# Kernel optimization log

Hardware: AMD Instinct MI355X
Metric: run time of the kernel (lower is better)

The kernel has to match this reference:

```python
import jax, jax.numpy as jnp
import numpy as np

B, C, OC, H, W = 2, 64, 128, 96, 96
HD, DI, N, R, K = C // 2, C, 16, 2, 4  # VSSBlock: hidden=C/2, d_inner=2*hidden=C, d_state, dt_rank, 4 scan dirs
EPS = 1e-5


def _conv(x, w, b, pad, groups=1):
    y = jax.lax.conv_general_dilated(x, w, (1, 1), pad, feature_group_count=groups,
                                     dimension_numbers=('NCHW', 'OIHW', 'NCHW'))
    return y + b[None, :, None, None]


def _ln(x, w, b):
    m = x.mean(-1, keepdims=True)
    v = x.var(-1, keepdims=True)
    return (x - m) * jax.lax.rsqrt(v + EPS) * w + b


def _selective_scan(xs, dts, Bs, Cs, A, D):
    # xs, dts: (B,K,DI,L); Bs, Cs: (B,K,N,L); A: (K,DI,N); D: (K,DI)
    dts = jax.nn.softplus(dts)

    def step(h, inp):
        u_t, dt_t, B_t, C_t = inp
        dA = jnp.exp(dt_t[..., None] * A)                         # (B,K,DI,N)
        h = dA * h + (dt_t * u_t)[..., None] * B_t[:, :, None, :]
        return h, jnp.einsum('bkdn,bkn->bkd', h, C_t)

    seq = (jnp.moveaxis(xs, -1, 0), jnp.moveaxis(dts, -1, 0),
           jnp.moveaxis(Bs, -1, 0), jnp.moveaxis(Cs, -1, 0))
    h0 = jnp.zeros(xs.shape[:3] + (A.shape[-1],), xs.dtype)
    _, ys = jax.lax.scan(step, h0, seq)
    return jnp.moveaxis(ys, 0, -1) + D[None, :, :, None] * xs


def _vss_block(x, ln_w, ln_b, in_w, conv_w, conv_b, xproj_w, dtproj_w, dtproj_b,
               A_logs, Ds, on_w, on_b, out_w):
    # x: (B,H,W,HD); VMamba SS2D with 4-direction cross-scan + residual
    b, hh, ww, _ = x.shape
    L = hh * ww
    h = _ln(x, ln_w, ln_b)
    xz = h @ in_w                                   # (B,H,W,2*DI)
    xp, z = jnp.split(xz, 2, axis=-1)
    xc = jnp.transpose(xp, (0, 3, 1, 2))            # (B,DI,H,W)
    xc = jax.nn.silu(_conv(xc, conv_w, conv_b, ((1, 1), (1, 1)), groups=DI))
    x_flat = xc.reshape(b, DI, L)
    x_wh = jnp.transpose(xc, (0, 1, 3, 2)).reshape(b, DI, L)
    x2 = jnp.stack([x_flat, x_wh], axis=1)
    xs = jnp.concatenate([x2, jnp.flip(x2, -1)], axis=1)      # (B,4,DI,L)
    x_dbl = jnp.einsum('bkdl,kcd->bkcl', xs, xproj_w)
    dts, Bs, Cs = jnp.split(x_dbl, [R, R + N], axis=2)
    dts = jnp.einsum('bkrl,kdr->bkdl', dts, dtproj_w) + dtproj_b[None, :, :, None]
    A = -jnp.exp(A_logs)
    ys = _selective_scan(xs, dts, Bs, Cs, A, Ds)              # (B,4,DI,L)
    inv = jnp.flip(ys[:, 2:4], -1)
    unwh = lambda t: jnp.transpose(t.reshape(b, DI, ww, hh), (0, 1, 3, 2)).reshape(b, DI, L)
    y = ys[:, 0] + inv[:, 0] + unwh(ys[:, 1]) + unwh(inv[:, 1])
    y = jnp.transpose(y.reshape(b, DI, hh, ww), (0, 2, 3, 1))
    y = _ln(y, on_w, on_b) * jax.nn.silu(z)
    return x + y @ out_w


def _forward(x, ms_dw33_w, ms_dw33_b, ms_in_w, ms_in_b, ms_scale,
             vss_ln_w, vss_ln_b, vss_in_w, vss_conv_w, vss_conv_b, vss_xproj_w,
             vss_dtproj_w, vss_dtproj_b, vss_A_logs, vss_Ds, vss_on_w, vss_on_b, vss_out_w,
             ma_conv_w, ma_conv_b, adw_h_w, adw_h_b, adw_w_w, adw_w_b,
             pw_w, pw_b, bn_w, bn_b, bn_mean, bn_var):
    vss = (vss_ln_w, vss_ln_b, vss_in_w, vss_conv_w, vss_conv_b, vss_xproj_w,
           vss_dtproj_w, vss_dtproj_b, vss_A_logs, vss_Ds, vss_on_w, vss_on_b, vss_out_w)
    # --- MambaSplit (shared VSSBlock applied to both channel halves) ---
    xd = _conv(x, ms_dw33_w, ms_dw33_b, ((1, 1), (1, 1)), groups=C)
    x1, x2 = jnp.split(xd, 2, axis=1)

    def branch(xp):
        y = _vss_block(jnp.transpose(xp, (0, 2, 3, 1)), *vss)
        return ms_scale * xp + jnp.transpose(y, (0, 3, 1, 2))

    xm = jnp.concatenate([branch(x1), branch(x2)], axis=1)
    m = xm.mean((2, 3), keepdims=True)
    v = xm.var((2, 3), keepdims=True)
    xm = (xm - m) * jax.lax.rsqrt(v + EPS) * ms_in_w[None, :, None, None] + ms_in_b[None, :, None, None]
    xm = jax.nn.leaky_relu(xm, 0.01)
    # --- MaxAvg (global avg+max pool -> 3x3 conv on 1x1 map -> sigmoid gate) ---
    pooled = jnp.concatenate([x.mean((2, 3), keepdims=True), x.max((2, 3), keepdims=True)], axis=1)
    gate = jax.nn.sigmoid(_conv(pooled, ma_conv_w, ma_conv_b, ((1, 1), (1, 1))))
    xs_ = xm + gate * x
    # --- AxialDW ---
    xs_ = xs_ + _conv(xs_, adw_h_w, adw_h_b, ((1, 1), (0, 0)), groups=C) \
              + _conv(xs_, adw_w_w, adw_w_b, ((0, 0), (1, 1)), groups=C)
    # --- BN (eval) + ReLU, 1x1 conv, 2x2 maxpool ---
    skip = jax.nn.relu((xs_ - bn_mean[None, :, None, None]) * jax.lax.rsqrt(bn_var[None, :, None, None] + EPS)
                       * bn_w[None, :, None, None] + bn_b[None, :, None, None])
    out = _conv(skip, pw_w, pw_b, ((0, 0), (0, 0)))
    down = jax.lax.reduce_window(out, -jnp.inf, jax.lax.max, (1, 1, 2, 2), (1, 1, 2, 2), 'VALID')
    return down, skip


def setup_inputs() -> dict:
    key = jax.random.key(0)
    ks = jax.random.split(key, 16)
    r = lambda i, shape, s=0.02: jax.random.normal(ks[i], shape, jnp.float32) * s
    return {
        'x': jax.random.normal(ks[0], (B, C, H, W), jnp.float32),
        'ms_dw33_w': r(1, (C, 1, 3, 3), 0.1), 'ms_dw33_b': jnp.zeros(C),
        'ms_in_w': jnp.ones(C), 'ms_in_b': jnp.zeros(C),
        'ms_scale': jnp.ones((1,)),
        'vss_ln_w': jnp.ones(HD), 'vss_ln_b': jnp.zeros(HD),
        'vss_in_w': r(2, (HD, 2 * DI)),
        'vss_conv_w': r(3, (DI, 1, 3, 3), 0.1), 'vss_conv_b': jnp.zeros(DI),
        'vss_xproj_w': r(4, (K, R + 2 * N, DI)),
        'vss_dtproj_w': r(5, (K, DI, R), 0.1), 'vss_dtproj_b': r(6, (K, DI), 0.1),
        'vss_A_logs': jnp.tile(jnp.log(jnp.arange(1, N + 1, dtype=jnp.float32)), (K, DI, 1)),
        'vss_Ds': jnp.ones((K, DI)),
        'vss_on_w': jnp.ones(DI), 'vss_on_b': jnp.zeros(DI),
        'vss_out_w': r(7, (DI, HD)),
        'ma_conv_w': r(8, (C, 2 * C, 3, 3), 0.05), 'ma_conv_b': jnp.zeros(C),
        'adw_h_w': r(9, (C, 1, 3, 1), 0.1), 'adw_h_b': jnp.zeros(C),
        'adw_w_w': r(10, (C, 1, 1, 3), 0.1), 'adw_w_b': jnp.zeros(C),
        'pw_w': r(11, (OC, C, 1, 1)), 'pw_b': jnp.zeros(OC),
        'bn_w': jnp.ones(C), 'bn_b': jnp.zeros(C),
        'bn_mean': jnp.zeros(C), 'bn_var': jnp.ones(C),
    }


def reference(x, ms_dw33_w, ms_dw33_b, ms_in_w, ms_in_b, ms_scale,
              vss_ln_w, vss_ln_b, vss_in_w, vss_conv_w, vss_conv_b, vss_xproj_w,
              vss_dtproj_w, vss_dtproj_b, vss_A_logs, vss_Ds, vss_on_w, vss_on_b, vss_out_w,
              ma_conv_w, ma_conv_b, adw_h_w, adw_h_b, adw_w_w, adw_w_b,
              pw_w, pw_b, bn_w, bn_b, bn_mean, bn_var):
    return _forward(x, ms_dw33_w, ms_dw33_b, ms_in_w, ms_in_b, ms_scale,
                    vss_ln_w, vss_ln_b, vss_in_w, vss_conv_w, vss_conv_b, vss_xproj_w,
                    vss_dtproj_w, vss_dtproj_b, vss_A_logs, vss_Ds, vss_on_w, vss_on_b, vss_out_w,
                    ma_conv_w, ma_conv_b, adw_h_w, adw_h_b, adw_w_w, adw_w_b,
                    pw_w, pw_b, bn_w, bn_b, bn_mean, bn_var)
```

## Files before the change

kernel.cpp:

```cpp
#include <hip/hip_runtime.h>
#include <hip/hip_bf16.h>

typedef __hip_bfloat16 bf16;
#define DEV __device__ __forceinline__

constexpr int B_ = 2, C_ = 64, H_ = 96, W_ = 96, L_ = 9216;
constexpr int HD_ = 32, DI_ = 64, N_ = 16, K_ = 4, BB_ = 4;
constexpr int OC_ = 128;
constexpr int CH_ = 384, CL_ = 24;
constexpr int SEGN = 32, SEGC = 12;
constexpr float EPSF = 1e-5f;
constexpr int DOWN_SZ = B_ * OC_ * 48 * 48;

typedef __attribute__((ext_vector_type(8))) short short8;
typedef __attribute__((ext_vector_type(4))) float f32x4;
typedef __attribute__((ext_vector_type(2))) float f32x2;

DEV float softplusf(float x) { return x > 15.f ? x : __logf(1.f + __expf(x)); }
DEV float b2f(bf16 v) { return __bfloat162float(v); }
DEV float lo16f(unsigned v) { return __uint_as_float(v << 16); }
DEV float hi16f(unsigned v) { return __uint_as_float(v & 0xffff0000u); }
DEV f32x2 pk2(unsigned w) { f32x2 r = {lo16f(w), hi16f(w)}; return r; }
DEV void unpk8(uint4 a, float* v) {
  v[0] = lo16f(a.x); v[1] = hi16f(a.x); v[2] = lo16f(a.y); v[3] = hi16f(a.y);
  v[4] = lo16f(a.z); v[5] = hi16f(a.z); v[6] = lo16f(a.w); v[7] = hi16f(a.w);
}
DEV void unpk(uint4 a, uint4 b, float* v) {
  unpk8(a, v); unpk8(b, v + 8);
}

__constant__ float kLogN[16] = {
  0.0f, 0.69314718f, 1.09861229f, 1.38629436f, 1.60943791f, 1.79175947f,
  1.94591015f, 2.07944154f, 2.19722458f, 2.30258509f, 2.39789527f,
  2.48490665f, 2.56494936f, 2.63905733f, 2.70805020f, 2.77258872f};

DEV void pow_tree2(float e1, f32x2* ep) {
  float e2 = e1 * e1;
  ep[0].x = e1; ep[0].y = e2;
  f32x2 b2v = {e2, e2};
  ep[1] = ep[0] * b2v;
  float e4 = ep[1].y;
  f32x2 b4v = {e4, e4};
  ep[2] = ep[0] * b4v;
  ep[3] = ep[1] * b4v;
  float e8 = ep[3].y;
  f32x2 b8v = {e8, e8};
  ep[4] = ep[0] * b8v;
  ep[5] = ep[1] * b8v;
  ep[6] = ep[2] * b8v;
  ep[7] = ep[3] * b8v;
}

DEV void pow_tree(float e1, float* ep) {
  float e2 = e1 * e1, e4 = e2 * e2, e8 = e4 * e4;
  float e3 = e2 * e1, e5 = e4 * e1, e6 = e4 * e2, e7 = e4 * e3;
  ep[0] = e1;  ep[1] = e2;  ep[2] = e3;  ep[3] = e4;
  ep[4] = e5;  ep[5] = e6;  ep[6] = e7;  ep[7] = e8;
  ep[8] = e8 * e1;  ep[9] = e8 * e2;  ep[10] = e8 * e3;  ep[11] = e8 * e4;
  ep[12] = e8 * e5; ep[13] = e8 * e6; ep[14] = e8 * e7;  ep[15] = e8 * e8;
}

__global__ __launch_bounds__(256, 4) void k_front(
    const float* __restrict__ x, const float* __restrict__ dw33w,
    const float* __restrict__ dw33b, const float* __restrict__ lnw,
    const float* __restrict__ lnb, const float* __restrict__ inw,
    const float* __restrict__ xpw, const float* __restrict__ alog,
    float* __restrict__ xd, bf16* __restrict__ xzAh, bf16* __restrict__ xzBh,
    bf16* __restrict__ wh, float* __restrict__ aux) {
  int bb = blockIdx.y, t = threadIdx.x;
  int b = bb & 1, co = (bb >> 1) * HD_;
  int idx0 = blockIdx.x * 32;
  if (bb == 0) {
    int i = blockIdx.x * 256 + t;
    if (i < 144 * 64) {
      int n = i >> 6;
      wh[i] = __float2bfloat16(n < 136 ? xpw[i] : 0.f);
    }
    if (blockIdx.x == 0) {
      int kd = t;
      const float* al = alog + kd * N_;
      float a0 = al[0];
      bool lin = true;
#pragma unroll
      for (int n = 1; n < N_; n++) lin = lin && (fabsf(al[n] - a0 - kLogN[n]) < 3e-5f);
      aux[kd] = -__expf(a0);
      aux[256 + kd] = lin ? 1.f : 0.f;
#pragma unroll
      for (int n = 0; n < N_; n++) aux[512 + kd * N_ + n] = -__expf(al[n]);
    }
  }
  __shared__ float xds[32 * 36];
  __shared__ float meanA[32], rstdA[32];
  for (int i = t; i < 1024; i += 256) {
    int cl = i >> 5, ii = i & 31;
    int sp = idx0 + ii, wi = sp % 96, hi = sp / 96;
    int cg = b * C_ + co + cl;
    float acc = dw33b[co + cl];
#pragma unroll
    for (int dy = -1; dy <= 1; dy++) {
      int hh = hi + dy; if (hh < 0 || hh >= H_) continue;
#pragma unroll
      for (int dx = -1; dx <= 1; dx++) {
        int ww = wi + dx; if (ww < 0 || ww >= W_) continue;
        acc = fmaf(x[(size_t)cg * L_ + sp + dy * 96 + dx],
                   dw33w[(co + cl) * 9 + (dy + 1) * 3 + (dx + 1)], acc);
      }
    }
    xds[cl * 36 + ii] = acc;
    xd[(size_t)cg * L_ + sp] = acc;
  }
  __syncthreads();
  if (t < 32) {
    float s = 0.f, sq = 0.f;
#pragma unroll
    for (int c = 0; c < 32; c++) { float v = xds[c * 36 + t]; s += v; sq = fmaf(v, v, sq); }
    float mean = s * (1.f / HD_);
    float var = sq * (1.f / HD_) - mean * mean;
    meanA[t] = mean; rstdA[t] = rsqrtf(var + EPSF);
  }
  __syncthreads();
  for (int i = t; i < 1024; i += 256) {
    int c = i >> 5, idx = i & 31;
    float v = xds[c * 36 + idx];
    xds[c * 36 + idx] = (v - meanA[idx]) * rstdA[idx] * lnw[c] + lnb[c];
  }
  __syncthreads();
  int oc = t & 127, g = t >> 7;
  float acc[16];
#pragma unroll
  for (int j = 0; j < 16; j++) acc[j] = 0.f;
  for (int c = 0; c < 32; c++) {
    float wv = inw[c * 128 + oc];
    const float4* row = reinterpret_cast<const float4*>(&xds[c * 36 + g * 16]);
#pragma unroll
    for (int j4 = 0; j4 < 4; j4++) {
      float4 xv = row[j4];
      acc[j4 * 4 + 0] = fmaf(xv.x, wv, acc[j4 * 4 + 0]);
      acc[j4 * 4 + 1] = fmaf(xv.y, wv, acc[j4 * 4 + 1]);
      acc[j4 * 4 + 2] = fmaf(xv.z, wv, acc[j4 * 4 + 2]);
      acc[j4 * 4 + 3] = fmaf(xv.w, wv, acc[j4 * 4 + 3]);
    }
  }
  int occ = oc & 63;
  if (oc < 64) {
#pragma unroll
    for (int j = 0; j < 16; j++)
      xzAh[(size_t)(bb * L_ + idx0 + g * 16 + j) * 64 + occ] = __float2bfloat16(acc[j]);
  } else {
#pragma unroll
    for (int j = 0; j < 16; j++)
      xzBh[(size_t)(bb * L_ + idx0 + g * 16 + j) * 64 + occ] = __float2bfloat16(acc[j]);
  }
}

__global__ void k_dwsilu(const bf16* __restrict__ xzAh, const float* __restrict__ cw,
                         const float* __restrict__ cb, bf16* __restrict__ xch,
                         bf16* __restrict__ xcht) {
  int t = blockIdx.x * 256 + threadIdx.x;
  int d = t & 63, idx = (t >> 6) % L_, bb = t / (L_ * DI_);
  int wi = idx % W_, hi = idx / W_;
  float acc = cb[d];
#pragma unroll
  for (int dy = -1; dy <= 1; dy++) {
    int hh = hi + dy; if (hh < 0 || hh >= H_) continue;
#pragma unroll
    for (int dx = -1; dx <= 1; dx++) {
      int ww = wi + dx; if (ww < 0 || ww >= W_) continue;
      acc = fmaf(b2f(xzAh[(size_t)(bb * L_ + hh * W_ + ww) * 64 + d]),
                 cw[d * 9 + (dy + 1) * 3 + (dx + 1)], acc);
    }
  }
  acc = acc / (1.f + __expf(-acc));
  bf16 v = __float2bfloat16(acc);
  xch[t] = v;
  int idx_t = wi * 96 + hi;
  xcht[((size_t)bb * L_ + idx_t) * DI_ + d] = v;
}

__global__ __launch_bounds__(256, 4) void k_xdbl_mfma(
    const bf16* __restrict__ xch, const bf16* __restrict__ wh,
    float* __restrict__ xdblB, bf16* __restrict__ xdblC) {
  int w = threadIdx.x >> 6, lane = threadIdx.x & 63;
  int bb = blockIdx.y;
  int mtile = blockIdx.x * 4 + w;
  int idx0 = mtile * 16;
  int m = lane & 15, quad = lane >> 4;
  const bf16* arow = xch + ((size_t)bb * L_ + idx0 + m) * 64 + quad * 8;
  short8 a0 = *reinterpret_cast<const short8*>(arow);
  short8 a1 = *reinterpret_cast<const short8*>(arow + 32);
  int ntb = blockIdx.z * 3;
#pragma unroll
  for (int it = 0; it < 3; it++) {
    int nt = ntb + it;
    int n = nt * 16 + m;
    const bf16* brow = wh + n * 64 + quad * 8;
    short8 b0 = *reinterpret_cast<const short8*>(brow);
    short8 b1 = *reinterpret_cast<const short8*>(brow + 32);
    f32x4 acc = {0.f, 0.f, 0.f, 0.f};
    acc = __builtin_amdgcn_mfma_f32_16x16x32_bf16(a0, b0, acc, 0, 0, 0);
    acc = __builtin_amdgcn_mfma_f32_16x16x32_bf16(a1, b1, acc, 0, 0, 0);
    if (n < 136) {
      int k4 = (n >= 102) ? 3 : (n >= 68) ? 2 : (n >= 34) ? 1 : 0;
      int c = n - k4 * 34;
#pragma unroll
      for (int i = 0; i < 4; i++) {
        int r = idx0 + quad * 4 + i;
        int hi2 = r / 96, wi2 = r - hi2 * 96;
        int tr = wi2 * 96 + hi2;
        int ls = (k4 == 0) ? r : (k4 == 1) ? tr : (k4 == 2) ? (L_ - 1 - r) : (L_ - 1 - tr);
        size_t row = (size_t)(bb * K_ + k4) * L_ + ls;
        if (c < 2)       xdblB[row * 12 + 8 + c] = acc[i];
        else if (c < 18) ((bf16*)(xdblB + row * 12))[c - 2] = __float2bfloat16(acc[i]);
        else             xdblC[row * 16 + (c - 18)] = __float2bfloat16(acc[i]);
      }
    }
  }
}

__global__ __launch_bounds__(256, 4) void k_scan1(
    const float* __restrict__ xdblB, const bf16* __restrict__ xch,
    const bf16* __restrict__ xcht, const float* __restrict__ dtw,
    const float* __restrict__ dtb, const float* __restrict__ aux,
    bf16* __restrict__ hbuf, float* __restrict__ ssum) {
  int w = threadIdx.x >> 6, d = threadIdx.x & 63;
  int bx = blockIdx.x;
  int chunk = bx * 4 + w, k = blockIdx.y, bb = blockIdx.z;
  const float* bB = xdblB + (size_t)(bb * K_ + k) * L_ * 12;
  __shared__ __align__(16) float sB[96 * 12];
  {
    const uint4* src = (const uint4*)(bB + (size_t)bx * 96 * 12);
    uint4* dst = (uint4*)sB;
    for (int i = threadIdx.x; i < 288; i += 256) dst[i] = src[i];
  }
  __syncthreads();
  float w0 = dtw[(k * DI_ + d) * 2 + 0], w1 = dtw[(k * DI_ + d) * 2 + 1];
  float bia = dtb[k * DI_ + d];
  float A1 = aux[k * 64 + d];
  bool chain = (__ballot(aux[256 + k * 64 + d] > 0.5f) == ~0ull);
  const bf16* ub = ((k & 1) ? xcht : xch) + (size_t)bb * L_ * DI_;
  int ls0 = chunk * CL_;
  int uidx0 = (k & 2) ? (L_ - 1 - ls0) : ls0;
  int ustep = (k & 2) ? -1 : 1;
  float S = 0.f;
  size_t base = (size_t)((bb * K_ + k) * CH_ + chunk) * DI_ + d;
  if (chain) {
    f32x2 h2[8];
#pragma unroll
    for (int i = 0; i < 8; i++) { h2[i].x = 0.f; h2[i].y = 0.f; }
#pragma unroll 4
    for (int s = 0; s < CL_; s++) {
      const float* p = sB + (w * CL_ + s) * 12;
      uint4 qb0 = *(const uint4*)p, qb1 = *(const uint4*)(p + 4);
      float t0 = p[8], t1 = p[9];
      float u = b2f(ub[(size_t)(uidx0 + s * ustep) * DI_ + d]);
      float dt = softplusf(fmaf(t0, w0, fmaf(t1, w1, bia)));
      S += dt;
      float du = dt * u;
      f32x2 du2 = {du, du};
      f32x2 ep2[8];
      pow_tree2(__expf(dt * A1), ep2);
      h2[0] = ep2[0] * h2[0] + du2 * pk2(qb0.x);
      h2[1] = ep2[1] * h2[1] + du2 * pk2(qb0.y);
      h2[2] = ep2[2] * h2[2] + du2 * pk2(qb0.z);
      h2[3] = ep2[3] * h2[3] + du2 * pk2(qb0.w);
      h2[4] = ep2[4] * h2[4] + du2 * pk2(qb1.x);
      h2[5] = ep2[5] * h2[5] + du2 * pk2(qb1.y);
      h2[6] = ep2[6] * h2[6] + du2 * pk2(qb1.z);
      h2[7] = ep2[7] * h2[7] + du2 * pk2(qb1.w);
    }
#pragma unroll
    for (int i = 0; i < 8; i++) {
      hbuf[base * N_ + 2 * i]     = __float2bfloat16(h2[i].x);
      hbuf[base * N_ + 2 * i + 1] = __float2bfloat16(h2[i].y);
    }
  } else {
    float h[N_];
#pragma unroll
    for (int n = 0; n < N_; n++) h[n] = 0.f;
    float A[N_];
#pragma unroll
    for (int n = 0; n < N_; n++) A[n] = aux[512 + (k * 64 + d) * N_ + n];
    for (int s = 0; s < CL_; s++) {
      const float* p = sB + (w * CL_ + s) * 12;
      uint4 qb0 = *(const uint4*)p, qb1 = *(const uint4*)(p + 4);
      float t0 = p[8], t1 = p[9];
      float u = b2f(ub[(size_t)(uidx0 + s * ustep) * DI_ + d]);
      float Bv[16];
      unpk(qb0, qb1, Bv);
      float dt = softplusf(fmaf(t0, w0, fmaf(t1, w1, bia)));
      S += dt;
      float du = dt * u;
#pragma unroll
      for (int n = 0; n < N_; n++) h[n] = fmaf(__expf(dt * A[n]), h[n], du * Bv[n]);
    }
#pragma unroll
    for (int n = 0; n < N_; n++) hbuf[base * N_ + n] = __float2bfloat16(h[n]);
  }
  ssum[base] = S;
}

__global__ __launch_bounds__(256, 4) void k_scan2a(
    const float* __restrict__ aux, const float* __restrict__ ssum,
    bf16* __restrict__ hbuf, float* __restrict__ cumS,
    float* __restrict__ segH, float* __restrict__ segS) {
  int t = blockIdx.x * 256 + threadIdx.x;
  int n = t & 15, d = (t >> 4) & 63, kk = (t >> 10) & 3, bb = (t >> 12) & 3, seg = t >> 14;
  float A = aux[512 + (kk * 64 + d) * N_ + n];
  size_t row = (size_t)(bb * K_ + kk) * CH_ * DI_ + d;
  float hp = 0.f, Sc = 0.f;
#pragma unroll 4
  for (int j = 0; j < SEGC; j++) {
    int c = seg * SEGC + j;
    size_t sb = row + (size_t)c * DI_;
    float S = ssum[sb];
    float hl = b2f(hbuf[sb * N_ + n]);
    hbuf[sb * N_ + n] = __float2bfloat16(hp);
    if (n == 0) cumS[sb] = Sc;
    hp = fmaf(__expf(A * S), hp, hl);
    Sc += S;
  }
  size_t sbase = (size_t)(bb * K_ + kk) * SEGN + seg;
  segH[(sbase * DI_ + d) * N_ + n] = hp;
  if (n == 0) segS[sbase * DI_ + d] = Sc;
}

__global__ void k_scan2b(const float* __restrict__ aux, float* __restrict__ segH,
                         const float* __restrict__ segS) {
  int t = blockIdx.x * 256 + threadIdx.x;
  int n = t & 15, d = (t >> 4) & 63, kk = (t >> 10) & 3, bb = t >> 12;
  float A = aux[512 + (kk * 64 + d) * N_ + n];
  float hp = 0.f;
  for (int seg = 0; seg < SEGN; seg++) {
    size_t sbase = (size_t)(bb * K_ + kk) * SEGN + seg;
    size_t si = (sbase * DI_ + d) * N_ + n;
    float H = segH[si];
    float E = __expf(A * segS[sbase * DI_ + d]);
    segH[si] = hp;
    hp = fmaf(E, hp, H);
  }
}

__global__ __launch_bounds__(256, 4) void k_scan3(
    const float* __restrict__ xdblB, const bf16* __restrict__ xdblC,
    const bf16* __restrict__ xch, const bf16* __restrict__ xcht,
    const float* __restrict__ dtw, const float* __restrict__ dtb,
    const float* __restrict__ Dsw, const float* __restrict__ aux,
    const bf16* __restrict__ hbuf, const float* __restrict__ cumS,
    const float* __restrict__ segH, bf16* __restrict__ ydir) {
  int w = threadIdx.x >> 6, d = threadIdx.x & 63;
  int bx = blockIdx.x;
  int chunk = bx * 4 + w, k = blockIdx.y, bb = blockIdx.z;
  const float* bB = xdblB + (size_t)(bb * K_ + k) * L_ * 12;
  const bf16* bC = xdblC + (size_t)(bb * K_ + k) * L_ * 16;
  __shared__ __align__(16) float sB[96 * 12];
  __shared__ __align__(16) bf16 sC[96 * 16];
  {
    const uint4* srcB = (const uint4*)(bB + (size_t)bx * 96 * 12);
    uint4* dstB = (uint4*)sB;
    for (int i = threadIdx.x; i < 288; i += 256) dstB[i] = srcB[i];
    const uint4* srcC = (const uint4*)(bC + (size_t)bx * 96 * 16);
    uint4* dstC = (uint4*)sC;
    if (threadIdx.x < 192) dstC[threadIdx.x] = srcC[threadIdx.x];
  }
  __syncthreads();
  float w0 = dtw[(k * DI_ + d) * 2 + 0], w1 = dtw[(k * DI_ + d) * 2 + 1];
  float bia = dtb[k * DI_ + d];
  float Dk = Dsw[k * DI_ + d];
  float A1 = aux[k * 64 + d];
  bool chain = (__ballot(aux[256 + k * 64 + d] > 0.5f) == ~0ull);
  size_t base = (size_t)((bb * K_ + k) * CH_ + chunk) * DI_ + d;
  int seg = chunk / SEGC;
  size_t sbase = (size_t)(bb * K_ + k) * SEGN + seg;
  float Sc = cumS[base];
  const bf16* ub = ((k & 1) ? xcht : xch) + (size_t)bb * L_ * DI_;
  bf16* yb = ydir + (size_t)(bb * K_ + k) * L_ * DI_;
  int ls0 = chunk * CL_;
  int uidx0 = (k & 2) ? (L_ - 1 - ls0) : ls0;
  int ustep = (k & 2) ? -1 : 1;
  const bf16* hb = hbuf + base * N_;
  const float* Hin = segH + (sbase * DI_ + d) * N_;
  if (chain) {
    f32x2 h2[8];
    {
      uint4 qh0 = *(const uint4*)hb, qh1 = *(const uint4*)(hb + 8);
      h2[0] = pk2(qh0.x); h2[1] = pk2(qh0.y); h2[2] = pk2(qh0.z); h2[3] = pk2(qh0.w);
      h2[4] = pk2(qh1.x); h2[5] = pk2(qh1.y); h2[6] = pk2(qh1.z); h2[7] = pk2(qh1.w);
      f32x2 ep2[8];
      pow_tree2(__expf(A1 * Sc), ep2);
#pragma unroll
      for (int i = 0; i < 8; i++)
        h2[i] = ep2[i] * (*(const f32x2*)(Hin + 2 * i)) + h2[i];
    }
#pragma unroll 2
    for (int s = 0; s < CL_; s++) {
      int lr = w * CL_ + s;
      const float* p = sB + lr * 12;
      uint4 qb0 = *(const uint4*)p, qb1 = *(const uint4*)(p + 4);
      float t0 = p[8], t1 = p[9];
      const uint4* cq = (const uint4*)(sC + lr * 16);
      uint4 qc0 = cq[0], qc1 = cq[1];
      float u = b2f(ub[(size_t)(uidx0 + s * ustep) * DI_ + d]);
      float dt = softplusf(fmaf(t0, w0, fmaf(t1, w1, bia)));
      float du = dt * u;
      f32x2 du2 = {du, du};
      f32x2 ep2[8];
      pow_tree2(__expf(dt * A1), ep2);
      f32x2 y2 = {0.f, 0.f};
      h2[0] = ep2[0] * h2[0] + du2 * pk2(qb0.x);  y2 = h2[0] * pk2(qc0.x) + y2;
      h2[1] = ep2[1] * h2[1] + du2 * pk2(qb0.y);  y2 = h2[1] * pk2(qc0.y) + y2;
      h2[2] = ep2[2] * h2[2] + du2 * pk2(qb0.z);  y2 = h2[2] * pk2(qc0.z) + y2;
      h2[3] = ep2[3] * h2[3] + du2 * pk2(qb0.w);  y2 = h2[3] * pk2(qc0.w) + y2;
      h2[4] = ep2[4] * h2[4] + du2 * pk2(qb1.x);  y2 = h2[4] * pk2(qc1.x) + y2;
      h2[5] = ep2[5] * h2[5] + du2 * pk2(qb1.y);  y2 = h2[5] * pk2(qc1.y) + y2;
      h2[6] = ep2[6] * h2[6] + du2 * pk2(qb1.z);  y2 = h2[6] * pk2(qc1.z) + y2;
      h2[7] = ep2[7] * h2[7] + du2 * pk2(qb1.w);  y2 = h2[7] * pk2(qc1.w) + y2;
      float y = fmaf(Dk, u, y2.x + y2.y);
      yb[(size_t)(ls0 + s) * DI_ + d] = __float2bfloat16(y);
    }
  } else {
    float h[N_];
    {
      uint4 qh0 = *(const uint4*)hb, qh1 = *(const uint4*)(hb + 8);
      unpk(qh0, qh1, h);
#pragma unroll
      for (int n = 0; n < N_; n++) {
        float A = aux[512 + (k * 64 + d) * N_ + n];
        h[n] = fmaf(__expf(A * Sc), Hin[n], h[n]);
      }
    }
    float A[N_];
#pragma unroll
    for (int n = 0; n < N_; n++) A[n] = aux[512 + (k * 64 + d) * N_ + n];
    for (int s = 0; s < CL_; s++) {
      int lr = w * CL_ + s;
      const float* p = sB + lr * 12;
      uint4 qb0 = *(const uint4*)p, qb1 = *(const uint4*)(p + 4);
      float t0 = p[8], t1 = p[9];
      const uint4* cq = (const uint4*)(sC + lr * 16);
      uint4 qc0 = cq[0], qc1 = cq[1];
      float u = b2f(ub[(size_t)(uidx0 + s * ustep) * DI_ + d]);
      float Bv[16], Cv[16];
      unpk(qb0, qb1, Bv); unpk(qc0, qc1, Cv);
      float dt = softplusf(fmaf(t0, w0, fmaf(t1, w1, bia)));
      float du = dt * u;
      float y = 0.f;
#pragma unroll
      for (int n = 0; n < N_; n++) {
        h[n] = fmaf(__expf(dt * A[n]), h[n], du * Bv[n]);
        y = fmaf(h[n], Cv[n], y);
      }
      y = fmaf(Dk, u, y);
      yb[(size_t)(ls0 + s) * DI_ + d] = __float2bfloat16(y);
    }
  }
}

__global__ void k_combine(const bf16* __restrict__ ydir, const bf16* __restrict__ xzBh,
                          const float* __restrict__ xd, const float* __restrict__ onw,
                          const float* __restrict__ onb, const float* __restrict__ outw,
                          const float* __restrict__ mssc, float* __restrict__ xm) {
  int w = threadIdx.x >> 6, d = threadIdx.x & 63;
  int idx = blockIdx.x * 4 + w, bb = blockIdx.y;
  int b = bb & 1, co = (bb >> 1) * HD_;
  int hii = idx / 96, wii = idx - hii * 96;
  int lt = wii * 96 + hii;
  const bf16* yd = ydir + (size_t)bb * K_ * L_ * DI_;
  float y = b2f(yd[((size_t)0 * L_ + idx) * DI_ + d])
          + b2f(yd[((size_t)1 * L_ + lt) * DI_ + d])
          + b2f(yd[((size_t)2 * L_ + (L_ - 1 - idx)) * DI_ + d])
          + b2f(yd[((size_t)3 * L_ + (L_ - 1 - lt)) * DI_ + d]);
  float s = y, sq = y * y;
#pragma unroll
  for (int m = 1; m < 64; m <<= 1) { s += __shfl_xor(s, m, 64); sq += __shfl_xor(sq, m, 64); }
  float mean = s * (1.f / DI_);
  float var = sq * (1.f / DI_) - mean * mean;
  float rstd = rsqrtf(var + EPSF);
  float yn = (y - mean) * rstd * onw[d] + onb[d];
  float z = b2f(xzBh[(size_t)(bb * L_ + idx) * 64 + d]);
  float g = yn * (z / (1.f + __expf(-z)));
  __shared__ float gs[4][DI_];
  gs[w][d] = g;
  __syncthreads();
  if (d < HD_) {
    float acc = 0.f;
#pragma unroll
    for (int dd = 0; dd < DI_; dd++) acc = fmaf(gs[w][dd], outw[dd * HD_ + d], acc);
    size_t xi = (size_t)(b * C_ + co + d) * L_ + idx;
    float xp = xd[xi];
    xm[xi] = mssc[0] * xp + xp + acc;
  }
}

__global__ __launch_bounds__(1024) void k_stats(
    const float* __restrict__ xm, const float* __restrict__ x,
    float* __restrict__ inm, float* __restrict__ inr,
    float* __restrict__ xmean, float* __restrict__ xmax) {
  int bc = blockIdx.x, t = threadIdx.x;
  const float* pm = xm + (size_t)bc * L_;
  const float* px = x + (size_t)bc * L_;
  float s = 0.f, sq = 0.f, xs = 0.f, mx = -1e30f;
  for (int i = t; i < L_; i += 1024) {
    float v = pm[i]; s += v; sq = fmaf(v, v, sq);
    float xv = px[i]; xs += xv; mx = fmaxf(mx, xv);
  }
  __shared__ float red[64];
#pragma unroll
  for (int m = 1; m < 64; m <<= 1) {
    s += __shfl_xor(s, m, 64); sq += __shfl_xor(sq, m, 64);
    xs += __shfl_xor(xs, m, 64); mx = fmaxf(mx, __shfl_xor(mx, m, 64));
  }
  int wid = t >> 6;
  if ((t & 63) == 0) { red[wid] = s; red[16 + wid] = sq; red[32 + wid] = xs; red[48 + wid] = mx; }
  __syncthreads();
  if (t == 0) {
    s = 0.f; sq = 0.f; xs = 0.f; mx = -1e30f;
#pragma unroll
    for (int i = 0; i < 16; i++) {
      s += red[i]; sq += red[16 + i]; xs += red[32 + i]; mx = fmaxf(mx, red[48 + i]);
    }
    float mean = s * (1.f / L_);
    float var = sq * (1.f / L_) - mean * mean;
    inm[bc] = mean;
    inr[bc] = rsqrtf(var + EPSF);
    xmean[bc] = xs * (1.f / L_);
    xmax[bc] = mx;
  }
}

__global__ void k_axbn(const float* __restrict__ xm, const float* __restrict__ x,
                       const float* __restrict__ inm, const float* __restrict__ inr,
                       const float* __restrict__ msw, const float* __restrict__ msb,
                       const float* __restrict__ xmean, const float* __restrict__ xmax,
                       const float* __restrict__ maw, const float* __restrict__ mab,
                       const float* __restrict__ hw, const float* __restrict__ hb,
                       const float* __restrict__ wwt, const float* __restrict__ wb,
                       const float* __restrict__ bnw, const float* __restrict__ bnb,
                       const float* __restrict__ bnm, const float* __restrict__ bnv,
                       float* __restrict__ skipo) {
  int t = blockIdx.x * 256 + threadIdx.x;
  int bc = t / L_, c = bc & 63, b = bc >> 6;
  __shared__ float gsh;
  if (threadIdx.x < 64) {
    int ic = threadIdx.x;
    float p = xmean[b * 64 + ic] * maw[(c * 128 + ic) * 9 + 4]
            + xmax[b * 64 + ic] * maw[(c * 128 + 64 + ic) * 9 + 4];
#pragma unroll
    for (int m = 1; m < 64; m <<= 1) p += __shfl_xor(p, m, 64);
    if (ic == 0) gsh = 1.f / (1.f + __expf(-(p + mab[c])));
  }
  __syncthreads();
  float gate = gsh, im = inm[bc], ir = inr[bc], mw = msw[c], mb = msb[c];
  int wi = t % W_, hi = (t / W_) % H_;
  auto xsv = [&](int tt) -> float {
    float v = xm[tt];
    v = (v - im) * ir * mw + mb;
    v = v > 0.f ? v : 0.01f * v;
    return v + gate * x[tt];
  };
  float a = xsv(t);
  float hacc = hb[c];
#pragma unroll
  for (int dy = -1; dy <= 1; dy++) {
    int hh = hi + dy; if (hh < 0 || hh >= H_) continue;
    hacc = fmaf(xsv(t + dy * W_), hw[c * 3 + dy + 1], hacc);
  }
  float wacc = wb[c];
#pragma unroll
  for (int dx = -1; dx <= 1; dx++) {
    int ww = wi + dx; if (ww < 0 || ww >= W_) continue;
    wacc = fmaf(xsv(t + dx), wwt[c * 3 + dx + 1], wacc);
  }
  float v = a + hacc + wacc;
  float sv = (v - bnm[c]) * rsqrtf(bnv[c] + EPSF) * bnw[c] + bnb[c];
  skipo[t] = fmaxf(sv, 0.f);
}

__global__ void k_pwpool(const float* __restrict__ skipo, const float* __restrict__ pww,
                         const float* __restrict__ pwb, float* __restrict__ down) {
  int h2 = blockIdx.x, b = blockIdx.y, t = threadIdx.x;
  int oc0 = blockIdx.z * 32;
  __shared__ float sk[64 * 192];
  for (int i = t; i < 64 * 192; i += 256) {
    int c = i / 192, rw = i % 192, r = rw / 96, wcol = rw % 96;
    sk[i] = skipo[((size_t)(b * C_ + c) * H_ + (2 * h2 + r)) * W_ + wcol];
  }
  __syncthreads();
  for (int o = t; o < 32 * 48; o += 256) {
    int oc = oc0 + o / 48, w2 = o % 48;
    float s0 = 0.f, s1 = 0.f, s2 = 0.f, s3 = 0.f;
#pragma unroll 8
    for (int c = 0; c < 64; c++) {
      float wv = pww[oc * 64 + c];
      const float* sp = &sk[c * 192 + 2 * w2];
      s0 = fmaf(sp[0], wv, s0);
      s1 = fmaf(sp[1], wv, s1);
      s2 = fmaf(sp[96], wv, s2);
      s3 = fmaf(sp[97], wv, s3);
    }
    float v = fmaxf(fmaxf(s0, s1), fmaxf(s2, s3)) + pwb[oc];
    down[((size_t)(b * OC_ + oc) * 48 + h2) * 48 + w2] = v;
  }
}

extern "C" void kernel_launch(void* const* d_in, const int* in_sizes, int n_in,
                              void* d_out, int out_size, void* d_ws, size_t ws_size,
                              hipStream_t stream) {
  const float* x     = (const float*)d_in[0];
  const float* dw33w = (const float*)d_in[1];
  const float* dw33b = (const float*)d_in[2];
  const float* msw   = (const float*)d_in[3];
  const float* msb   = (const float*)d_in[4];
  const float* mssc  = (const float*)d_in[5];
  const float* lnw   = (const float*)d_in[6];
  const float* lnb   = (const float*)d_in[7];
  const float* inw   = (const float*)d_in[8];
  const float* cw    = (const float*)d_in[9];
  const float* cb    = (const float*)d_in[10];
  const float* xpw   = (const float*)d_in[11];
  const float* dtw   = (const float*)d_in[12];
  const float* dtb   = (const float*)d_in[13];
  const float* alog  = (const float*)d_in[14];
  const float* Dsw   = (const float*)d_in[15];
  const float* onw   = (const float*)d_in[16];
  const float* onb   = (const float*)d_in[17];
  const float* outw  = (const float*)d_in[18];
  const float* maw   = (const float*)d_in[19];
  const float* mab   = (const float*)d_in[20];
  const float* ahw   = (const float*)d_in[21];
  const float* ahb   = (const float*)d_in[22];
  const float* aww   = (const float*)d_in[23];
  const float* awb   = (const float*)d_in[24];
  const float* pww   = (const float*)d_in[25];
  const float* pwb   = (const float*)d_in[26];
  const float* bnw   = (const float*)d_in[27];
  const float* bnb   = (const float*)d_in[28];
  const float* bnm   = (const float*)d_in[29];
  const float* bnv   = (const float*)d_in[30];

  float* ws = (float*)d_ws;
  float* xd    = ws;
  float* hreg  = xd + 1179648;
  bf16*  hbuf  = (bf16*)hreg;
  bf16*  xzAh  = (bf16*)hreg;
  bf16*  xzBh  = (bf16*)(hreg + 12582912);
  float* xdblB = hreg + 12582912 + 1179648;
  bf16*  xdblC = (bf16*)(xdblB + 1769472);
  float* ssum  = xdblB + 1769472 + 1179648;
  bf16*  ydir  = (bf16*)(ssum + 1572864);
  float* xmR   = ssum + 1572864 + 4718592;
  bf16*  xch   = (bf16*)xmR;
  float* xm    = xmR;
  float* st    = xmR + 1179648;
  float* inm = st, *inr = st + 128, *xmean = st + 256, *xmaxv = st + 384;
  float* aux   = st + 512;
  bf16*  wh    = (bf16*)(aux + 4608);
  float* cumS  = aux + 4608 + 4608;
  float* segH  = cumS + 1572864;
  float* segS  = segH + 524288;
  bf16*  xcht  = (bf16*)(segS + 32768);

  float* outp = (float*)d_out;
  float* down = outp;
  float* skipo = outp + DOWN_SZ;

  dim3 b256(256);
  int nEl = B_ * C_ * L_;

  k_front<<<dim3(L_ / 32, BB_), b256, 0, stream>>>(x, dw33w, dw33b, lnw, lnb, inw,
                                                   xpw, alog, xd, xzAh, xzBh, wh, aux);
  k_dwsilu<<<dim3(BB_ * L_ * DI_ / 256), b256, 0, stream>>>(xzAh, cw, cb, xch, xcht);
  k_xdbl_mfma<<<dim3(L_ / 64, BB_, 3), b256, 0, stream>>>(xch, wh, xdblB, xdblC);
  k_scan1<<<dim3(CH_ / 4, K_, BB_), b256, 0, stream>>>(xdblB, xch, xcht, dtw, dtb, aux, hbuf, ssum);
  k_scan2a<<<dim3(BB_ * K_ * SEGN * DI_ * N_ / 256), b256, 0, stream>>>(aux, ssum, hbuf, cumS, segH, segS);
  k_scan2b<<<dim3(BB_ * K_ * DI_ * N_ / 256), b256, 0, stream>>>(aux, segH, segS);
  k_scan3<<<dim3(CH_ / 4, K_, BB_), b256, 0, stream>>>(xdblB, xdblC, xch, xcht, dtw, dtb, Dsw,
                                                      aux, hbuf, cumS, segH, ydir);
  k_combine<<<dim3(L_ / 4, BB_), b256, 0, stream>>>(ydir, xzBh, xd, onw, onb, outw, mssc, xm);
  k_stats<<<dim3(B_ * C_), dim3(1024), 0, stream>>>(xm, x, inm, inr, xmean, xmaxv);
  k_axbn<<<dim3((nEl + 255) / 256), b256, 0, stream>>>(xm, x, inm, inr, msw, msb, xmean, xmaxv,
                                                      maw, mab, ahw, ahb, aww, awb,
                                                      bnw, bnb, bnm, bnv, skipo);
  k_pwpool<<<dim3(48, B_, 4), b256, 0, stream>>>(skipo, pww, pwb, down);
}
```

Measured before the change: 303.2 us.

## Store scan B/C projections in fp32, prefetch u, and stage skip stencil in LDS

Changes the B and C projection buffers from packed bf16 to fp32 (B row padded to 20 floats), so the scan kernels read values directly from shared memory without unpacking. The scan loops are fully unrolled and the per-step u values are preloaded into registers before the recurrence. The skip/BN kernel now computes the normalized activation once per element into an LDS tile with a halo, rather than recomputing it for each stencil tap. Workspace offsets are compacted to match. The cost is roughly double the global and LDS traffic for B/C and higher register pressure from the unrolled loops.

```diff
diff --git a/kernel.cpp b/kernel.cpp
--- a/kernel.cpp
+++ b/kernel.cpp
@@ -9,6 +9,7 @@
 constexpr int OC_ = 128;
 constexpr int CH_ = 384, CL_ = 24;
 constexpr int SEGN = 32, SEGC = 12;
+constexpr int BROW = 20;
 constexpr float EPSF = 1e-5f;
 constexpr int DOWN_SZ = B_ * OC_ * 48 * 48;
 
@@ -51,15 +52,6 @@
   ep[7] = ep[3] * b8v;
 }
 
-DEV void pow_tree(float e1, float* ep) {
-  float e2 = e1 * e1, e4 = e2 * e2, e8 = e4 * e4;
-  float e3 = e2 * e1, e5 = e4 * e1, e6 = e4 * e2, e7 = e4 * e3;
-  ep[0] = e1;  ep[1] = e2;  ep[2] = e3;  ep[3] = e4;
-  ep[4] = e5;  ep[5] = e6;  ep[6] = e7;  ep[7] = e8;
-  ep[8] = e8 * e1;  ep[9] = e8 * e2;  ep[10] = e8 * e3;  ep[11] = e8 * e4;
-  ep[12] = e8 * e5; ep[13] = e8 * e6; ep[14] = e8 * e7;  ep[15] = e8 * e8;
-}
-
 __global__ __launch_bounds__(256, 4) void k_front(
     const float* __restrict__ x, const float* __restrict__ dw33w,
     const float* __restrict__ dw33b, const float* __restrict__ lnw,
@@ -179,7 +171,7 @@
 
 __global__ __launch_bounds__(256, 4) void k_xdbl_mfma(
     const bf16* __restrict__ xch, const bf16* __restrict__ wh,
-    float* __restrict__ xdblB, bf16* __restrict__ xdblC) {
+    float* __restrict__ xdblB, float* __restrict__ xdblC) {
   int w = threadIdx.x >> 6, lane = threadIdx.x & 63;
   int bb = blockIdx.y;
   int mtile = blockIdx.x * 4 + w;
@@ -209,9 +201,9 @@
         int tr = wi2 * 96 + hi2;
         int ls = (k4 == 0) ? r : (k4 == 1) ? tr : (k4 == 2) ? (L_ - 1 - r) : (L_ - 1 - tr);
         size_t row = (size_t)(bb * K_ + k4) * L_ + ls;
-        if (c < 2)       xdblB[row * 12 + 8 + c] = acc[i];
-        else if (c < 18) ((bf16*)(xdblB + row * 12))[c - 2] = __float2bfloat16(acc[i]);
-        else             xdblC[row * 16 + (c - 18)] = __float2bfloat16(acc[i]);
+        if (c < 2)       xdblB[row * BROW + 16 + c] = acc[i];
+        else if (c < 18) xdblB[row * BROW + (c - 2)] = acc[i];
+        else             xdblC[row * 16 + (c - 18)] = acc[i];
       }
     }
   }
@@ -225,12 +217,12 @@
   int w = threadIdx.x >> 6, d = threadIdx.x & 63;
   int bx = blockIdx.x;
   int chunk = bx * 4 + w, k = blockIdx.y, bb = blockIdx.z;
-  const float* bB = xdblB + (size_t)(bb * K_ + k) * L_ * 12;
-  __shared__ __align__(16) float sB[96 * 12];
+  const float* bB = xdblB + (size_t)(bb * K_ + k) * L_ * BROW;
+  __shared__ __align__(16) float sB[96 * BROW];
   {
-    const uint4* src = (const uint4*)(bB + (size_t)bx * 96 * 12);
+    const uint4* src = (const uint4*)(bB + (size_t)bx * 96 * BROW);
     uint4* dst = (uint4*)sB;
-    for (int i = threadIdx.x; i < 288; i += 256) dst[i] = src[i];
+    for (int i = threadIdx.x; i < 480; i += 256) dst[i] = src[i];
   }
   __syncthreads();
   float w0 = dtw[(k * DI_ + d) * 2 + 0], w1 = dtw[(k * DI_ + d) * 2 + 1];
@@ -244,29 +236,25 @@
   float S = 0.f;
   size_t base = (size_t)((bb * K_ + k) * CH_ + chunk) * DI_ + d;
   if (chain) {
+    float uv[CL_];
+    const bf16* up = ub + (size_t)uidx0 * DI_ + d;
+#pragma unroll
+    for (int s = 0; s < CL_; s++) uv[s] = b2f(up[s * ustep * DI_]);
     f32x2 h2[8];
 #pragma unroll
     for (int i = 0; i < 8; i++) { h2[i].x = 0.f; h2[i].y = 0.f; }
-#pragma unroll 4
+#pragma unroll
     for (int s = 0; s < CL_; s++) {
-      const float* p = sB + (w * CL_ + s) * 12;
-      uint4 qb0 = *(const uint4*)p, qb1 = *(const uint4*)(p + 4);
-      float t0 = p[8], t1 = p[9];
-      float u = b2f(ub[(size_t)(uidx0 + s * ustep) * DI_ + d]);
-      float dt = softplusf(fmaf(t0, w0, fmaf(t1, w1, bia)));
+      const float* p = sB + (w * CL_ + s) * BROW;
+      float dt = softplusf(fmaf(p[16], w0, fmaf(p[17], w1, bia)));
       S += dt;
-      float du = dt * u;
+      float du = dt * uv[s];
       f32x2 du2 = {du, du};
       f32x2 ep2[8];
       pow_tree2(__expf(dt * A1), ep2);
-      h2[0] = ep2[0] * h2[0] + du2 * pk2(qb0.x);
-      h2[1] = ep2[1] * h2[1] + du2 * pk2(qb0.y);
-      h2[2] = ep2[2] * h2[2] + du2 * pk2(qb0.z);
-      h2[3] = ep2[3] * h2[3] + du2 * pk2(qb0.w);
-      h2[4] = ep2[4] * h2[4] + du2 * pk2(qb1.x);
-      h2[5] = ep2[5] * h2[5] + du2 * pk2(qb1.y);
-      h2[6] = ep2[6] * h2[6] + du2 * pk2(qb1.z);
-      h2[7] = ep2[7] * h2[7] + du2 * pk2(qb1.w);
+#pragma unroll
+      for (int i = 0; i < 8; i++)
+        h2[i] = ep2[i] * h2[i] + du2 * (*(const f32x2*)(p + 2 * i));
     }
 #pragma unroll
     for (int i = 0; i < 8; i++) {
@@ -281,17 +269,13 @@
 #pragma unroll
     for (int n = 0; n < N_; n++) A[n] = aux[512 + (k * 64 + d) * N_ + n];
     for (int s = 0; s < CL_; s++) {
-      const float* p = sB + (w * CL_ + s) * 12;
-      uint4 qb0 = *(const uint4*)p, qb1 = *(const uint4*)(p + 4);
-      float t0 = p[8], t1 = p[9];
+      const float* p = sB + (w * CL_ + s) * BROW;
       float u = b2f(ub[(size_t)(uidx0 + s * ustep) * DI_ + d]);
-      float Bv[16];
-      unpk(qb0, qb1, Bv);
-      float dt = softplusf(fmaf(t0, w0, fmaf(t1, w1, bia)));
+      float dt = softplusf(fmaf(p[16], w0, fmaf(p[17], w1, bia)));
       S += dt;
       float du = dt * u;
 #pragma unroll
-      for (int n = 0; n < N_; n++) h[n] = fmaf(__expf(dt * A[n]), h[n], du * Bv[n]);
+      for (int n = 0; n < N_; n++) h[n] = fmaf(__expf(dt * A[n]), h[n], du * p[n]);
     }
 #pragma unroll
     for (int n = 0; n < N_; n++) hbuf[base * N_ + n] = __float2bfloat16(h[n]);
@@ -341,7 +325,7 @@
 }
 
 __global__ __launch_bounds__(256, 4) void k_scan3(
-    const float* __restrict__ xdblB, const bf16* __restrict__ xdblC,
+    const float* __restrict__ xdblB, const float* __restrict__ xdblC,
     const bf16* __restrict__ xch, const bf16* __restrict__ xcht,
     const float* __restrict__ dtw, const float* __restrict__ dtb,
     const float* __restrict__ Dsw, const float* __restrict__ aux,
@@ -350,17 +334,17 @@
   int w = threadIdx.x >> 6, d = threadIdx.x & 63;
   int bx = blockIdx.x;
   int chunk = bx * 4 + w, k = blockIdx.y, bb = blockIdx.z;
-  const float* bB = xdblB + (size_t)(bb * K_ + k) * L_ * 12;
-  const bf16* bC = xdblC + (size_t)(bb * K_ + k) * L_ * 16;
-  __shared__ __align__(16) float sB[96 * 12];
-  __shared__ __align__(16) bf16 sC[96 * 16];
+  const float* bB = xdblB + (size_t)(bb * K_ + k) * L_ * BROW;
+  const float* bC = xdblC + (size_t)(bb * K_ + k) * L_ * 16;
+  __shared__ __align__(16) float sB[96 * BROW];
+  __shared__ __align__(16) float sC[96 * 16];
   {
-    const uint4* srcB = (const uint4*)(bB + (size_t)bx * 96 * 12);
+    const uint4* srcB = (const uint4*)(bB + (size_t)bx * 96 * BROW);
     uint4* dstB = (uint4*)sB;
-    for (int i = threadIdx.x; i < 288; i += 256) dstB[i] = srcB[i];
+    for (int i = threadIdx.x; i < 480; i += 256) dstB[i] = srcB[i];
     const uint4* srcC = (const uint4*)(bC + (size_t)bx * 96 * 16);
     uint4* dstC = (uint4*)sC;
-    if (threadIdx.x < 192) dstC[threadIdx.x] = srcC[threadIdx.x];
+    for (int i = threadIdx.x; i < 384; i += 256) dstC[i] = srcC[i];
   }
   __syncthreads();
   float w0 = dtw[(k * DI_ + d) * 2 + 0], w1 = dtw[(k * DI_ + d) * 2 + 1];
@@ -380,6 +364,10 @@
   const bf16* hb = hbuf + base * N_;
   const float* Hin = segH + (sbase * DI_ + d) * N_;
   if (chain) {
+    float uv[CL_];
+    const bf16* up = ub + (size_t)uidx0 * DI_ + d;
+#pragma unroll
+    for (int s = 0; s < CL_; s++) uv[s] = b2f(up[s * ustep * DI_]);
     f32x2 h2[8];
     {
       uint4 qh0 = *(const uint4*)hb, qh1 = *(const uint4*)(hb + 8);
@@ -391,30 +379,23 @@
       for (int i = 0; i < 8; i++)
         h2[i] = ep2[i] * (*(const f32x2*)(Hin + 2 * i)) + h2[i];
     }
-#pragma unroll 2
+#pragma unroll
     for (int s = 0; s < CL_; s++) {
       int lr = w * CL_ + s;
-      const float* p = sB + lr * 12;
-      uint4 qb0 = *(const uint4*)p, qb1 = *(const uint4*)(p + 4);
-      float t0 = p[8], t1 = p[9];
-      const uint4* cq = (const uint4*)(sC + lr * 16);
-      uint4 qc0 = cq[0], qc1 = cq[1];
-      float u = b2f(ub[(size_t)(uidx0 + s * ustep) * DI_ + d]);
-      float dt = softplusf(fmaf(t0, w0, fmaf(t1, w1, bia)));
-      float du = dt * u;
+      const float* p = sB + lr * BROW;
+      const float* pc = sC + lr * 16;
+      float dt = softplusf(fmaf(p[16], w0, fmaf(p[17], w1, bia)));
+      float du = dt * uv[s];
       f32x2 du2 = {du, du};
       f32x2 ep2[8];
       pow_tree2(__expf(dt * A1), ep2);
       f32x2 y2 = {0.f, 0.f};
-      h2[0] = ep2[0] * h2[0] + du2 * pk2(qb0.x);  y2 = h2[0] * pk2(qc0.x) + y2;
-      h2[1] = ep2[1] * h2[1] + du2 * pk2(qb0.y);  y2 = h2[1] * pk2(qc0.y) + y2;
-      h2[2] = ep2[2] * h2[2] + du2 * pk2(qb0.z);  y2 = h2[2] * pk2(qc0.z) + y2;
-      h2[3] = ep2[3] * h2[3] + du2 * pk2(qb0.w);  y2 = h2[3] * pk2(qc0.w) + y2;
-      h2[4] = ep2[4] * h2[4] + du2 * pk2(qb1.x);  y2 = h2[4] * pk2(qc1.x) + y2;
-      h2[5] = ep2[5] * h2[5] + du2 * pk2(qb1.y);  y2 = h2[5] * pk2(qc1.y) + y2;
-      h2[6] = ep2[6] * h2[6] + du2 * pk2(qb1.z);  y2 = h2[6] * pk2(qc1.z) + y2;
-      h2[7] = ep2[7] * h2[7] + du2 * pk2(qb1.w);  y2 = h2[7] * pk2(qc1.w) + y2;
-      float y = fmaf(Dk, u, y2.x + y2.y);
+#pragma unroll
+      for (int i = 0; i < 8; i++) {
+        h2[i] = ep2[i] * h2[i] + du2 * (*(const f32x2*)(p + 2 * i));
+        y2 = h2[i] * (*(const f32x2*)(pc + 2 * i)) + y2;
+      }
+      float y = fmaf(Dk, uv[s], y2.x + y2.y);
       yb[(size_t)(ls0 + s) * DI_ + d] = __float2bfloat16(y);
     }
   } else {
@@ -433,21 +414,16 @@
     for (int n = 0; n < N_; n++) A[n] = aux[512 + (k * 64 + d) * N_ + n];
     for (int s = 0; s < CL_; s++) {
       int lr = w * CL_ + s;
-      const float* p = sB + lr * 12;
-      uint4 qb0 = *(const uint4*)p, qb1 = *(const uint4*)(p + 4);
-      float t0 = p[8], t1 = p[9];
-      const uint4* cq = (const uint4*)(sC + lr * 16);
-      uint4 qc0 = cq[0], qc1 = cq[1];
+      const float* p = sB + lr * BROW;
+      const float* pc = sC + lr * 16;
       float u = b2f(ub[(size_t)(uidx0 + s * ustep) * DI_ + d]);
-      float Bv[16], Cv[16];
-      unpk(qb0, qb1, Bv); unpk(qc0, qc1, Cv);
-      float dt = softplusf(fmaf(t0, w0, fmaf(t1, w1, bia)));
+      float dt = softplusf(fmaf(p[16], w0, fmaf(p[17], w1, bia)));
       float du = dt * u;
       float y = 0.f;
 #pragma unroll
       for (int n = 0; n < N_; n++) {
-        h[n] = fmaf(__expf(dt * A[n]), h[n], du * Bv[n]);
-        y = fmaf(h[n], Cv[n], y);
+        h[n] = fmaf(__expf(dt * A[n]), h[n], du * p[n]);
+        y = fmaf(h[n], pc[n], y);
       }
       y = fmaf(Dk, u, y);
       yb[(size_t)(ls0 + s) * DI_ + d] = __float2bfloat16(y);
@@ -537,9 +513,12 @@
                        const float* __restrict__ bnw, const float* __restrict__ bnb,
                        const float* __restrict__ bnm, const float* __restrict__ bnv,
                        float* __restrict__ skipo) {
-  int t = blockIdx.x * 256 + threadIdx.x;
-  int bc = t / L_, c = bc & 63, b = bc >> 6;
+  constexpr int NEL = B_ * C_ * L_;
+  int t0 = blockIdx.x * 256;
+  int t = t0 + threadIdx.x;
+  int bc = t0 / L_, c = bc & 63, b = bc >> 6;
   __shared__ float gsh;
+  __shared__ float sxs[448];
   if (threadIdx.x < 64) {
     int ic = threadIdx.x;
     float p = xmean[b * 64 + ic] * maw[(c * 128 + ic) * 9 + 4]
@@ -550,25 +529,29 @@
   }
   __syncthreads();
   float gate = gsh, im = inm[bc], ir = inr[bc], mw = msw[c], mb = msb[c];
-  int wi = t % W_, hi = (t / W_) % H_;
-  auto xsv = [&](int tt) -> float {
+  for (int i = threadIdx.x; i < 448; i += 256) {
+    int tt = t0 - 96 + i;
+    tt = tt < 0 ? 0 : (tt >= NEL ? NEL - 1 : tt);
     float v = xm[tt];
     v = (v - im) * ir * mw + mb;
     v = v > 0.f ? v : 0.01f * v;
-    return v + gate * x[tt];
-  };
-  float a = xsv(t);
+    sxs[i] = v + gate * x[tt];
+  }
+  __syncthreads();
+  int li = 96 + threadIdx.x;
+  int wi = t % W_, hi = (t / W_) % H_;
+  float a = sxs[li];
   float hacc = hb[c];
 #pragma unroll
   for (int dy = -1; dy <= 1; dy++) {
     int hh = hi + dy; if (hh < 0 || hh >= H_) continue;
-    hacc = fmaf(xsv(t + dy * W_), hw[c * 3 + dy + 1], hacc);
+    hacc = fmaf(sxs[li + dy * 96], hw[c * 3 + dy + 1], hacc);
   }
   float wacc = wb[c];
 #pragma unroll
   for (int dx = -1; dx <= 1; dx++) {
     int ww = wi + dx; if (ww < 0 || ww >= W_) continue;
-    wacc = fmaf(xsv(t + dx), wwt[c * 3 + dx + 1], wacc);
+    wacc = fmaf(sxs[li + dx], wwt[c * 3 + dx + 1], wacc);
   }
   float v = a + hacc + wacc;
   float sv = (v - bnm[c]) * rsqrtf(bnv[c] + EPSF) * bnw[c] + bnb[c];
@@ -642,12 +625,12 @@
   float* hreg  = xd + 1179648;
   bf16*  hbuf  = (bf16*)hreg;
   bf16*  xzAh  = (bf16*)hreg;
-  bf16*  xzBh  = (bf16*)(hreg + 12582912);
-  float* xdblB = hreg + 12582912 + 1179648;
-  bf16*  xdblC = (bf16*)(xdblB + 1769472);
-  float* ssum  = xdblB + 1769472 + 1179648;
-  bf16*  ydir  = (bf16*)(ssum + 1572864);
-  float* xmR   = ssum + 1572864 + 4718592;
+  bf16*  xzBh  = (bf16*)(hreg + 1179648);
+  float* xdblB = hreg + 1179648 + 1179648;
+  float* xdblC = xdblB + 2949120;
+  float* ssum  = xdblC + 2359296;
+  bf16*  ydir  = (bf16*)(ssum + 393216);
+  float* xmR   = ssum + 393216 + 4718592;
   bf16*  xch   = (bf16*)xmR;
   float* xm    = xmR;
   float* st    = xmR + 1179648;
@@ -655,7 +638,7 @@
   float* aux   = st + 512;
   bf16*  wh    = (bf16*)(aux + 4608);
   float* cumS  = aux + 4608 + 4608;
-  float* segH  = cumS + 1572864;
+  float* segH  = cumS + 393216;
   float* segS  = segH + 524288;
   bf16*  xcht  = (bf16*)(segS + 32768);
 
```

New measurement: 293.4 us. 1.03x faster.
